# Optimization experiments

Measured on AMD Instinct MI355X. Metric: run time of the kernel, lower is better.

The kernel has to match this reference:

```python
import math
import jax, jax.numpy as jnp
import numpy as np

KEY_SIZE = 128
VALUE_SIZE = 128


def setup_inputs() -> dict:
    key = jax.random.key(0)
    # channels = value_size + 2*key_size = 384
    x = jax.random.normal(key, (8, VALUE_SIZE + 2 * KEY_SIZE, 32, 32), dtype=jnp.float32)
    return {"x": x}


def _tokens(t):
    # [B, C, H, W] -> [B*H*W, C]  (matches view/transpose/view in torch code)
    B, C = t.shape[0], t.shape[1]
    return t.reshape(B, C, -1).transpose(0, 2, 1).reshape(-1, C)


def reference(x) -> jnp.ndarray:
    B, C, H, W = x.shape
    value = _tokens(x[:, :VALUE_SIZE])                      # [N, V]
    key_t = _tokens(x[:, VALUE_SIZE:VALUE_SIZE + KEY_SIZE])  # [N, K]
    query = _tokens(x[:, VALUE_SIZE + KEY_SIZE:])            # [N, K]
    # Global N x N attention over all batch*spatial positions (faithful to source)
    weight = (query @ key_t.T) / math.sqrt(KEY_SIZE)         # [N, N]
    attention = jax.nn.softmax(weight, axis=1) @ value      # [N, V]
    out = attention.reshape(B, H * W, VALUE_SIZE).transpose(0, 2, 1)
    return out.reshape(B, VALUE_SIZE, H, W)
```

## Files before the change

### kernel.cpp

```cpp
#include <hip/hip_runtime.h>
#include <hip/hip_bf16.h>
#include <stdint.h>

#define N_TOK 8192
#define DDIM  128

typedef _Float16 half2v __attribute__((ext_vector_type(2)));
typedef _Float16 half4v __attribute__((ext_vector_type(4)));
typedef _Float16 half8v __attribute__((ext_vector_type(8)));
typedef __fp16  fp16x2 __attribute__((ext_vector_type(2)));
typedef float f32x4 __attribute__((ext_vector_type(4)));
typedef half4v half4_ma __attribute__((may_alias));
typedef half8v half8_ma __attribute__((may_alias));
typedef float4 float4_ma __attribute__((may_alias));

#define MFMA32 __builtin_amdgcn_mfma_f32_16x16x32_f16

#define QSCALE (0.08838834764831845f * 1.4426950408889634f)

__device__ __forceinline__ half2v pkrtz(float a, float b) {
  return __builtin_bit_cast(half2v, __builtin_amdgcn_cvt_pkrtz(a, b));
}

#if __has_builtin(__builtin_amdgcn_fdot2)
__device__ __forceinline__ float dot2acc(half2v a, float c) {
  const fp16x2 ones = {(__fp16)1.f, (__fp16)1.f};
  return __builtin_amdgcn_fdot2(__builtin_bit_cast(fp16x2, a), ones, c, false);
}
#else
__device__ __forceinline__ float dot2acc(half2v a, float c) {
  return c + (float)a.x + (float)a.y;
}
#endif

__device__ __forceinline__ void gload_lds16(const _Float16* g, _Float16* l) {
  __builtin_amdgcn_global_load_lds(
      (const __attribute__((address_space(1))) void*)g,
      (__attribute__((address_space(3))) void*)l, 16, 0, 0);
}

__global__ void prep_all(const float* __restrict__ x,
                         _Float16* __restrict__ Qf, _Float16* __restrict__ Kf,
                         _Float16* __restrict__ Vt) {
  __shared__ float t[32][33];
  const int blk = blockIdx.x, tid = threadIdx.x;
  if (blk < 2048) {
    const int pt = blk & 31, ct = (blk >> 5) & 3, z = blk >> 7;
    const int b = z >> 1, isQ = z & 1;
    const int c0 = (isQ ? 256 : 128) + ct * 32;
    const int p0 = pt * 32;
    const int tx = tid & 31, ty0 = tid >> 5;
    const float* src = x + ((size_t)b * 384 + c0) * 1024 + p0;
#pragma unroll
    for (int i = 0; i < 4; ++i)
      t[ty0 + i * 8][tx] = src[(ty0 + i * 8) * 1024 + tx];
    __syncthreads();
    _Float16* dst = isQ ? Qf : Kf;
    const float sc = isQ ? QSCALE : 1.f;
#pragma unroll
    for (int i = 0; i < 4; ++i) {
      const int ty = ty0 + i * 8;
      dst[((size_t)b * 1024 + p0 + ty) * DDIM + ct * 32 + tx] = (_Float16)(t[tx][ty] * sc);
    }
  } else {
    const int i4 = ((blk - 2048) * 256 + tid) * 4;
    const int v = i4 >> 13, n = i4 & 8191;
    const int b = n >> 10, p = n & 1023;
    const float4 s = *(const float4_ma*)(x + ((size_t)b * 384 + v) * 1024 + p);
    half4v h; h.x = (_Float16)s.x; h.y = (_Float16)s.y; h.z = (_Float16)s.z; h.w = (_Float16)s.w;
    *(half4_ma*)(Vt + (size_t)v * N_TOK + b * 1024 + p) = h;
  }
}

template<int KS>
__global__ __launch_bounds__(256, 2) void flash_attn(
    const _Float16* __restrict__ Qf, const _Float16* __restrict__ Kf,
    const _Float16* __restrict__ Vt, _Float16* __restrict__ Opart,
    float* __restrict__ Lsum) {
  alignas(16) __shared__ _Float16 lds[16384];

  const int tid = threadIdx.x;
  const int w = tid >> 6, lane = tid & 63;
  const int quad = lane >> 4, l16 = lane & 15;
  const int blk = blockIdx.x;
  const int ks = (KS == 16) ? (((blk & 7) << 1) | (blk >> 8)) : (blk & 7);
  const int kp = N_TOK / KS;
  const int chunks = kp >> 5;
  const int k0 = ks * kp;
  const int q0 = ((blk >> 3) & 31) * 256;

  half8v qf[4][4];
#pragma unroll
  for (int qt = 0; qt < 4; ++qt) {
    const _Float16* qp = Qf + (size_t)(q0 + w * 64 + qt * 16 + l16) * DDIM + quad * 8;
#pragma unroll
    for (int kb = 0; kb < 4; ++kb) qf[qt][kb] = *(const half8_ma*)(qp + kb * 32);
  }

  f32x4 O[4][8];
#pragma unroll
  for (int qt = 0; qt < 4; ++qt)
#pragma unroll
    for (int vb = 0; vb < 8; ++vb) O[qt][vb] = (f32x4){0.f, 0.f, 0.f, 0.f};
  float ls[4] = {0.f, 0.f, 0.f, 0.f};

  const _Float16* srcK[2];
  const _Float16* srcV[2];
  int slotK[2], slotV[2];
#pragma unroll
  for (int j = 0; j < 2; ++j) {
    const int i = w * 2 + j;
    srcK[j] = Kf + (size_t)(k0 + (lane & 31)) * DDIM + (i * 2 + (lane >> 5)) * 8;
    slotK[j] = i * 512;
    const int v = i * 16 + (lane >> 2);
    const int lp = (lane & 3) ^ ((v >> 1) & 3);
    srcV[j] = Vt + (size_t)v * N_TOK + k0 + lp * 8;
    slotV[j] = 4096 + i * 512;
  }

#pragma unroll
  for (int j = 0; j < 2; ++j) {
    gload_lds16(srcK[j], lds + slotK[j]);
    gload_lds16(srcV[j], lds + slotV[j]);
  }

  const int sw = (l16 >> 1) & 3;
  for (int ch = 0; ch < chunks; ++ch) {
    __syncthreads();
    _Float16* buf = lds + (ch & 1) * 8192;
    if (ch + 1 < chunks) {
      _Float16* nbuf = lds + ((ch + 1) & 1) * 8192;
      const int adv = (ch + 1) * 32;
#pragma unroll
      for (int j = 0; j < 2; ++j) {
        gload_lds16(srcK[j] + (size_t)adv * DDIM, nbuf + slotK[j]);
        gload_lds16(srcV[j] + adv, nbuf + slotV[j]);
      }
    }
    const _Float16* Ksh = buf;
    const _Float16* Vsh = buf + 4096;

    f32x4 S[4][2];
#pragma unroll
    for (int qt = 0; qt < 4; ++qt)
#pragma unroll
      for (int cb = 0; cb < 2; ++cb) S[qt][cb] = (f32x4){0.f, 0.f, 0.f, 0.f};
#pragma unroll
    for (int kb = 0; kb < 4; ++kb) {
#pragma unroll
      for (int cb = 0; cb < 2; ++cb) {
        half8v kf = *(const half8_ma*)(Ksh + ((kb * 4 + quad) * 256 + (cb * 16 + l16) * 8));
#pragma unroll
        for (int qt = 0; qt < 4; ++qt)
          S[qt][cb] = MFMA32(kf, qf[qt][kb], S[qt][cb], 0, 0, 0);
      }
    }

    half8v P8[4];
#pragma unroll
    for (int qt = 0; qt < 4; ++qt) {
      const float a0 = __builtin_amdgcn_exp2f(S[qt][0][0]);
      const float a1 = __builtin_amdgcn_exp2f(S[qt][0][1]);
      const float a2 = __builtin_amdgcn_exp2f(S[qt][0][2]);
      const float a3 = __builtin_amdgcn_exp2f(S[qt][0][3]);
      const float b0 = __builtin_amdgcn_exp2f(S[qt][1][0]);
      const float b1 = __builtin_amdgcn_exp2f(S[qt][1][1]);
      const float b2 = __builtin_amdgcn_exp2f(S[qt][1][2]);
      const float b3 = __builtin_amdgcn_exp2f(S[qt][1][3]);
      half2v pa0 = pkrtz(a0, a1), pa1 = pkrtz(a2, a3);
      half2v pb0 = pkrtz(b0, b1), pb1 = pkrtz(b2, b3);
      ls[qt] = dot2acc(pa0, dot2acc(pa1, dot2acc(pb0, dot2acc(pb1, ls[qt]))));
      half4v lo = __builtin_shufflevector(pa0, pa1, 0, 1, 2, 3);
      half4v hi = __builtin_shufflevector(pb0, pb1, 0, 1, 2, 3);
      P8[qt] = __builtin_shufflevector(lo, hi, 0, 1, 2, 3, 4, 5, 6, 7);
    }

    const int pp1 = (quad >> 1) ^ sw;
    const int pp2 = pp1 ^ 2;
    const int hh = (quad & 1) * 4;
#pragma unroll
    for (int vb = 0; vb < 8; ++vb) {
      const int v = vb * 16 + l16;
      half4v lo = *(const half4_ma*)(Vsh + v * 32 + pp1 * 8 + hh);
      half4v hi = *(const half4_ma*)(Vsh + v * 32 + pp2 * 8 + hh);
      half8v vf = __builtin_shufflevector(lo, hi, 0, 1, 2, 3, 4, 5, 6, 7);
#pragma unroll
      for (int qt = 0; qt < 4; ++qt)
        O[qt][vb] = MFMA32(vf, P8[qt], O[qt][vb], 0, 0, 0);
    }
  }

#pragma unroll
  for (int qt = 0; qt < 4; ++qt) {
    ls[qt] += __shfl_xor(ls[qt], 16, 64);
    ls[qt] += __shfl_xor(ls[qt], 32, 64);
  }
#pragma unroll
  for (int qt = 0; qt < 4; ++qt) {
    const float rl = 1.f / ls[qt];
    const int q = q0 + w * 64 + qt * 16 + l16;
#pragma unroll
    for (int vb = 0; vb < 8; ++vb) {
#pragma unroll
      for (int r = 0; r < 4; ++r) {
        const int v = vb * 16 + quad * 4 + r;
        Opart[((size_t)ks * DDIM + v) * N_TOK + q] = (_Float16)(O[qt][vb][r] * rl);
      }
    }
  }
  if (lane < 16) {
#pragma unroll
    for (int qt = 0; qt < 4; ++qt)
      Lsum[(size_t)ks * N_TOK + q0 + w * 64 + qt * 16 + lane] = ls[qt];
  }
}

__global__ void combine_kernel(const _Float16* __restrict__ Opart,
                               const float* __restrict__ Lsum,
                               float* __restrict__ out, int KS) {
  const int o4 = (blockIdx.x * 256 + threadIdx.x) * 4;
  const int b = o4 >> 17, v = (o4 >> 10) & 127, p = o4 & 1023;
  const int q = (b << 10) | p;
  float4 num = make_float4(0.f, 0.f, 0.f, 0.f);
  float4 den = make_float4(0.f, 0.f, 0.f, 0.f);
  for (int s = 0; s < KS; ++s) {
    const float4 l = *(const float4_ma*)(Lsum + (size_t)s * N_TOK + q);
    const half4v ov = *(const half4_ma*)(Opart + ((size_t)s * DDIM + v) * N_TOK + q);
    num.x += l.x * (float)ov.x; num.y += l.y * (float)ov.y;
    num.z += l.z * (float)ov.z; num.w += l.w * (float)ov.w;
    den.x += l.x; den.y += l.y; den.z += l.z; den.w += l.w;
  }
  *(float4_ma*)(out + o4) =
      make_float4(num.x / den.x, num.y / den.y, num.z / den.z, num.w / den.w);
}

extern "C" void kernel_launch(void* const* d_in, const int* in_sizes, int n_in,
                              void* d_out, int out_size, void* d_ws, size_t ws_size,
                              hipStream_t stream) {
  const float* x = (const float*)d_in[0];
  float* out = (float*)d_out;
  char* ws = (char*)d_ws;

  const size_t need16 = (6u << 20) + 16 * (2u << 20) + (size_t)16 * N_TOK * 4;
  const int KS = (ws_size >= need16) ? 16 : 8;

  _Float16* Qf    = (_Float16*)(ws);
  _Float16* Kf    = (_Float16*)(ws + (2u << 20));
  _Float16* Vt    = (_Float16*)(ws + (4u << 20));
  _Float16* Opart = (_Float16*)(ws + (6u << 20));
  float*    Lsum  = (float*)(ws + (6u << 20) + (size_t)KS * (2u << 20));

  prep_all<<<dim3(3072), dim3(256), 0, stream>>>(x, Qf, Kf, Vt);
  if (KS == 16) {
    flash_attn<16><<<dim3(512), dim3(256), 0, stream>>>(Qf, Kf, Vt, Opart, Lsum);
  } else {
    flash_attn<8><<<dim3(256), dim3(256), 0, stream>>>(Qf, Kf, Vt, Opart, Lsum);
  }
  combine_kernel<<<dim3(1024), dim3(256), 0, stream>>>(Opart, Lsum, out, KS);
}
```

Before: 108.0 us.

## Load K and V fragments directly from global memory, dropping LDS staging

Removes the double-buffered global-to-LDS async loads and the per-chunk barrier. Each wave now reads its K and V MFMA operands straight from global memory, relying on L1/L2 caching. The V transpose in the prep kernel writes a permuted per-32-key panel layout, so each lane can fetch its 8-half V fragment with a single 16-byte load. This trades LDS reuse across the four waves for more redundant global/L1 traffic and exposed load latency, since there is no explicit prefetch and the loop is not unrolled.

```diff
diff --git a/kernel.cpp b/kernel.cpp
--- a/kernel.cpp
+++ b/kernel.cpp
@@ -32,12 +32,6 @@
   return c + (float)a.x + (float)a.y;
 }
 #endif
-
-__device__ __forceinline__ void gload_lds16(const _Float16* g, _Float16* l) {
-  __builtin_amdgcn_global_load_lds(
-      (const __attribute__((address_space(1))) void*)g,
-      (__attribute__((address_space(3))) void*)l, 16, 0, 0);
-}
 
 __global__ void prep_all(const float* __restrict__ x,
                          _Float16* __restrict__ Qf, _Float16* __restrict__ Kf,
@@ -68,7 +62,10 @@
     const int b = n >> 10, p = n & 1023;
     const float4 s = *(const float4_ma*)(x + ((size_t)b * 384 + v) * 1024 + p);
     half4v h; h.x = (_Float16)s.x; h.y = (_Float16)s.y; h.z = (_Float16)s.z; h.w = (_Float16)s.w;
-    *(half4_ma*)(Vt + (size_t)v * N_TOK + b * 1024 + p) = h;
+    const int key = (b << 10) + p;
+    const int panel = key >> 5, w = key & 31;
+    const int slot = (w < 16) ? ((w >> 2) << 3) : ((((w - 16) >> 2) << 3) + 4);
+    *(half4_ma*)(Vt + (size_t)v * N_TOK + panel * 32 + slot) = h;
   }
 }
 
@@ -77,8 +74,6 @@
     const _Float16* __restrict__ Qf, const _Float16* __restrict__ Kf,
     const _Float16* __restrict__ Vt, _Float16* __restrict__ Opart,
     float* __restrict__ Lsum) {
-  alignas(16) __shared__ _Float16 lds[16384];
-
   const int tid = threadIdx.x;
   const int w = tid >> 6, lane = tid & 63;
   const int quad = lane >> 4, l16 = lane & 15;
@@ -104,41 +99,12 @@
     for (int vb = 0; vb < 8; ++vb) O[qt][vb] = (f32x4){0.f, 0.f, 0.f, 0.f};
   float ls[4] = {0.f, 0.f, 0.f, 0.f};
 
-  const _Float16* srcK[2];
-  const _Float16* srcV[2];
-  int slotK[2], slotV[2];
-#pragma unroll
-  for (int j = 0; j < 2; ++j) {
-    const int i = w * 2 + j;
-    srcK[j] = Kf + (size_t)(k0 + (lane & 31)) * DDIM + (i * 2 + (lane >> 5)) * 8;
-    slotK[j] = i * 512;
-    const int v = i * 16 + (lane >> 2);
-    const int lp = (lane & 3) ^ ((v >> 1) & 3);
-    srcV[j] = Vt + (size_t)v * N_TOK + k0 + lp * 8;
-    slotV[j] = 4096 + i * 512;
-  }
-
-#pragma unroll
-  for (int j = 0; j < 2; ++j) {
-    gload_lds16(srcK[j], lds + slotK[j]);
-    gload_lds16(srcV[j], lds + slotV[j]);
-  }
-
-  const int sw = (l16 >> 1) & 3;
+  const _Float16* Kbase = Kf + (size_t)(k0 + l16) * DDIM + quad * 8;
+  const _Float16* Vbase = Vt + k0 + quad * 8;
+
+#pragma unroll 1
   for (int ch = 0; ch < chunks; ++ch) {
-    __syncthreads();
-    _Float16* buf = lds + (ch & 1) * 8192;
-    if (ch + 1 < chunks) {
-      _Float16* nbuf = lds + ((ch + 1) & 1) * 8192;
-      const int adv = (ch + 1) * 32;
-#pragma unroll
-      for (int j = 0; j < 2; ++j) {
-        gload_lds16(srcK[j] + (size_t)adv * DDIM, nbuf + slotK[j]);
-        gload_lds16(srcV[j] + adv, nbuf + slotV[j]);
-      }
-    }
-    const _Float16* Ksh = buf;
-    const _Float16* Vsh = buf + 4096;
+    const int kk = ch * 32;
 
     f32x4 S[4][2];
 #pragma unroll
@@ -149,7 +115,7 @@
     for (int kb = 0; kb < 4; ++kb) {
 #pragma unroll
       for (int cb = 0; cb < 2; ++cb) {
-        half8v kf = *(const half8_ma*)(Ksh + ((kb * 4 + quad) * 256 + (cb * 16 + l16) * 8));
+        half8v kf = *(const half8_ma*)(Kbase + (size_t)(kk + cb * 16) * DDIM + kb * 32);
 #pragma unroll
         for (int qt = 0; qt < 4; ++qt)
           S[qt][cb] = MFMA32(kf, qf[qt][kb], S[qt][cb], 0, 0, 0);
@@ -175,15 +141,10 @@
       P8[qt] = __builtin_shufflevector(lo, hi, 0, 1, 2, 3, 4, 5, 6, 7);
     }
 
-    const int pp1 = (quad >> 1) ^ sw;
-    const int pp2 = pp1 ^ 2;
-    const int hh = (quad & 1) * 4;
 #pragma unroll
     for (int vb = 0; vb < 8; ++vb) {
       const int v = vb * 16 + l16;
-      half4v lo = *(const half4_ma*)(Vsh + v * 32 + pp1 * 8 + hh);
-      half4v hi = *(const half4_ma*)(Vsh + v * 32 + pp2 * 8 + hh);
-      half8v vf = __builtin_shufflevector(lo, hi, 0, 1, 2, 3, 4, 5, 6, 7);
+      half8v vf = *(const half8_ma*)(Vbase + (size_t)v * N_TOK + kk);
 #pragma unroll
       for (int qt = 0; qt < 4; ++qt)
         O[qt][vb] = MFMA32(vf, P8[qt], O[qt][vb], 0, 0, 0);
```

After: 143.1 us. 1.32x slower.
